# Kernel optimization log

Measured on AMD Instinct MI355X. Metric: run time of the kernel, lower is better.

## Reference

```python
import jax, jax.numpy as jnp
import numpy as np

B, T, K = 256, 512, 128


def setup_inputs() -> dict:
    key = jax.random.key(0)
    k1, k2, k3, k4 = jax.random.split(key, 4)
    logits = jax.random.normal(k1, (B, T, K), dtype=jnp.float32)
    labels = jax.random.randint(k2, (B, T), 0, K, dtype=jnp.int32)
    seq_lens = jax.random.randint(k3, (B,), 1, T + 1, dtype=jnp.int32)
    trans = jax.random.uniform(k4, (K, K), dtype=jnp.float32)
    return {"logits": logits, "labels": labels, "seq_lens": seq_lens, "trans": trans}


def _crf_neg_log_likelihood(logits, labels, seq_lens, trans):
    # logits: [B,T,K], labels: [B,T] int, seq_lens: [B] int, trans: [K,K]
    Bb, Tt, Kk = logits.shape
    mask = (jnp.arange(Tt)[None, :] < seq_lens[:, None])  # [B,T] bool

    # ---- gold sequence score ----
    unary = jnp.take_along_axis(logits, labels[..., None].astype(jnp.int32), axis=-1)[..., 0]  # [B,T]
    unary_score = jnp.sum(jnp.where(mask, unary, 0.0), axis=-1)  # [B]
    pair = trans[labels[:, :-1], labels[:, 1:]]  # [B,T-1]
    pair_score = jnp.sum(jnp.where(mask[:, 1:], pair, 0.0), axis=-1)  # [B]
    score = unary_score + pair_score  # [B]

    # ---- log partition via forward algorithm (lax.scan over time) ----
    alpha0 = logits[:, 0]  # [B,K]
    xs = (jnp.swapaxes(logits[:, 1:], 0, 1), jnp.swapaxes(mask[:, 1:], 0, 1))  # [T-1,B,K],[T-1,B]

    def step(alpha, x):
        logit_t, m_t = x
        # alpha[:, :, None] + trans[None] : [B, K_prev, K_next]
        new = jax.nn.logsumexp(alpha[:, :, None] + trans[None, :, :], axis=1) + logit_t
        alpha = jnp.where(m_t[:, None], new, alpha)
        return alpha, None

    alpha, _ = jax.lax.scan(step, alpha0, xs)
    log_z = jax.nn.logsumexp(alpha, axis=-1)  # [B]

    log_likelihood = score - log_z
    return jnp.sum(-log_likelihood)  # scalar, matches tf.reduce_sum(-ll)


def reference(logits, labels, seq_lens, trans):
    return _crf_neg_log_likelihood(logits, labels, seq_lens, trans)
```

## Files before the change

kernel.cpp:

```cpp
#include <hip/hip_runtime.h>

#define Bdim 256
#define Tdim 512
#define Kdim 128
#define NT   512

#define BAR() asm volatile("s_waitcnt lgkmcnt(0)\n\ts_barrier" ::: "memory")

template <int CTRL>
__device__ __forceinline__ float dpp_add(float v) {
    int r = __builtin_amdgcn_update_dpp(0, __float_as_int(v), CTRL, 0xF, 0xF, true);
    return v + __int_as_float(r);
}

__global__ __launch_bounds__(NT, 1) void crf_nll_kernel(
    const float* __restrict__ logits,
    const int*   __restrict__ labels,
    const int*   __restrict__ seq_lens,
    const float* __restrict__ trans,
    float* __restrict__ out)
{
    const int b   = blockIdx.x;
    const int tid = threadIdx.x;
    const int j4  = tid >> 4;
    const int g   = tid & 15;
    const int cj  = 4 * j4 + (g & 3);
    const int L   = seq_lens[b];

    __shared__ float pbuf[2][Kdim];
    __shared__ float sred[NT / 64];
    __shared__ float ared[NT / 64];

    const int*   lab_b   = labels + (size_t)b * Tdim;
    const float* logit_b = logits + (size_t)b * Tdim * Kdim;

    float e[2][4][4];
    #pragma unroll
    for (int ii = 0; ii < 2; ++ii) {
        const int f = (g << 1) + (((g >> 2) & 1) ^ ii);
        #pragma unroll
        for (int ci = 0; ci < 4; ++ci) {
            const float4 tr =
                *(const float4*)&trans[(size_t)(4 * f + ci) * Kdim + 4 * j4];
            e[ii][ci][0] = __expf(tr.x);
            e[ii][ci][1] = __expf(tr.y);
            e[ii][ci][2] = __expf(tr.z);
            e[ii][ci][3] = __expf(tr.w);
        }
    }
    #pragma unroll
    for (int ii = 0; ii < 2; ++ii)
        #pragma unroll
        for (int ci = 0; ci < 4; ++ci)
            #pragma unroll
            for (int c = 0; c < 4; ++c)
                asm volatile("" : "+v"(e[ii][ci][c]));

    float s = 0.f;
    {
        const int t = tid;
        if (t < L) {
            const int lb = lab_b[t];
            s = logit_b[(size_t)t * Kdim + lb];
            if (t >= 1) s += trans[lab_b[t - 1] * Kdim + lb];
        }
    }
    #pragma unroll
    for (int o = 32; o > 0; o >>= 1) s += __shfl_down(s, o, 64);
    if ((tid & 63) == 0) sred[tid >> 6] = s;

    float a = 0.f, off = 0.f;
    if (g < 4) {
        a = __expf(logit_b[cj]);
        pbuf[0][cj] = a;
    }
    int cb = 0;
    __syncthreads();

    float score = 0.f;
    if (tid == 0) {
        #pragma unroll
        for (int w = 0; w < NT / 64; ++w) score += sred[w];
    }

    float curl[8], nxtl[8];
    #pragma unroll
    for (int u = 0; u < 8; ++u) {
        const int tt = 1 + u;
        curl[u] = (tt < Tdim) ? logit_b[(size_t)tt * Kdim + cj] : 0.f;
    }

    for (int tb = 1; tb < L; tb += 8) {
        #pragma unroll
        for (int u = 0; u < 8; ++u) {
            const int tt = tb + 8 + u;
            nxtl[u] = (tt < Tdim) ? logit_b[(size_t)tt * Kdim + cj] : 0.f;
        }
        #pragma unroll
        for (int u = 0; u < 8; ++u) {
            const int t = tb + u;
            if (t < L) {
                const float4* p4 = (const float4*)pbuf[cb];
                const float p0  = pbuf[cb][0];
                const float lp0 = __logf(p0);
                const float sc  = __expf(curl[u] - lp0);
                float acc0 = 0.f, acc1 = 0.f, acc2 = 0.f, acc3 = 0.f;
                #pragma unroll
                for (int ii = 0; ii < 2; ++ii) {
                    const float4 p = p4[(g << 1) + (((g >> 2) & 1) ^ ii)];
                    acc0 = fmaf(p.x, e[ii][0][0], acc0);
                    acc1 = fmaf(p.x, e[ii][0][1], acc1);
                    acc2 = fmaf(p.x, e[ii][0][2], acc2);
                    acc3 = fmaf(p.x, e[ii][0][3], acc3);
                    acc0 = fmaf(p.y, e[ii][1][0], acc0);
                    acc1 = fmaf(p.y, e[ii][1][1], acc1);
                    acc2 = fmaf(p.y, e[ii][1][2], acc2);
                    acc3 = fmaf(p.y, e[ii][1][3], acc3);
                    acc0 = fmaf(p.z, e[ii][2][0], acc0);
                    acc1 = fmaf(p.z, e[ii][2][1], acc1);
                    acc2 = fmaf(p.z, e[ii][2][2], acc2);
                    acc3 = fmaf(p.z, e[ii][2][3], acc3);
                    acc0 = fmaf(p.w, e[ii][3][0], acc0);
                    acc1 = fmaf(p.w, e[ii][3][1], acc1);
                    acc2 = fmaf(p.w, e[ii][3][2], acc2);
                    acc3 = fmaf(p.w, e[ii][3][3], acc3);
                }
                off += lp0;
                acc0 = dpp_add<0xB1>(acc0); acc0 = dpp_add<0x4E>(acc0);
                acc0 = dpp_add<0x124>(acc0); acc0 = dpp_add<0x128>(acc0);
                acc1 = dpp_add<0xB1>(acc1); acc1 = dpp_add<0x4E>(acc1);
                acc1 = dpp_add<0x124>(acc1); acc1 = dpp_add<0x128>(acc1);
                acc2 = dpp_add<0xB1>(acc2); acc2 = dpp_add<0x4E>(acc2);
                acc2 = dpp_add<0x124>(acc2); acc2 = dpp_add<0x128>(acc2);
                acc3 = dpp_add<0xB1>(acc3); acc3 = dpp_add<0x4E>(acc3);
                acc3 = dpp_add<0x124>(acc3); acc3 = dpp_add<0x128>(acc3);
                float sel  = (g & 1) ? acc1 : acc0;
                float selh = (g & 1) ? acc3 : acc2;
                sel = (g & 2) ? selh : sel;
                const float anew = sel * sc;
                if (g < 4) {
                    a = anew;
                    pbuf[cb ^ 1][cj] = anew;
                }
                cb ^= 1;
                BAR();
            }
        }
        #pragma unroll
        for (int u = 0; u < 8; ++u) curl[u] = nxtl[u];
    }

    float as = (g < 4) ? a : 0.f;
    #pragma unroll
    for (int o = 32; o > 0; o >>= 1) as += __shfl_down(as, o, 64);
    if ((tid & 63) == 0) ared[tid >> 6] = as;
    __syncthreads();
    if (tid == 0) {
        float tot = 0.f;
        #pragma unroll
        for (int w = 0; w < NT / 64; ++w) tot += ared[w];
        const float logz = off + __logf(tot);
        atomicAdd(out, logz - score);
    }
}

extern "C" void kernel_launch(void* const* d_in, const int* in_sizes, int n_in,
                              void* d_out, int out_size, void* d_ws, size_t ws_size,
                              hipStream_t stream) {
    const float* logits   = (const float*)d_in[0];
    const int*   labels   = (const int*)d_in[1];
    const int*   seq_lens = (const int*)d_in[2];
    const float* trans    = (const float*)d_in[3];
    float* out = (float*)d_out;

    (void)hipMemsetAsync(out, 0, sizeof(float), stream);
    crf_nll_kernel<<<dim3(Bdim), dim3(NT), 0, stream>>>(
        logits, labels, seq_lens, trans, out);
}
```

Before: 273.3 us.

## Double block size so each thread computes two output states instead of four

Raises threads per block from 512 to 1024. Each 16-lane group now covers 2 next-states instead of 4, which halves the per-thread FMA and DPP reduction chain in every serial time step. The logit prefetch depth drops from 8 to 4 steps. In exchange, each barrier now synchronises 16 wavefronts instead of 8, shared-memory broadcast reads double, and the register-pinning asm hints are removed.

```diff
diff --git a/kernel.cpp b/kernel.cpp
--- a/kernel.cpp
+++ b/kernel.cpp
@@ -3,7 +3,7 @@
 #define Bdim 256
 #define Tdim 512
 #define Kdim 128
-#define NT   512
+#define NT   1024
 
 #define BAR() asm volatile("s_waitcnt lgkmcnt(0)\n\ts_barrier" ::: "memory")
 
@@ -22,9 +22,9 @@
 {
     const int b   = blockIdx.x;
     const int tid = threadIdx.x;
-    const int j4  = tid >> 4;
+    const int jc  = tid >> 4;
     const int g   = tid & 15;
-    const int cj  = 4 * j4 + (g & 3);
+    const int cj  = 2 * jc + (g & 1);
     const int L   = seq_lens[b];
 
     __shared__ float pbuf[2][Kdim];
@@ -34,27 +34,18 @@
     const int*   lab_b   = labels + (size_t)b * Tdim;
     const float* logit_b = logits + (size_t)b * Tdim * Kdim;
 
-    float e[2][4][4];
+    float e[2][4][2];
     #pragma unroll
     for (int ii = 0; ii < 2; ++ii) {
         const int f = (g << 1) + (((g >> 2) & 1) ^ ii);
         #pragma unroll
         for (int ci = 0; ci < 4; ++ci) {
-            const float4 tr =
-                *(const float4*)&trans[(size_t)(4 * f + ci) * Kdim + 4 * j4];
+            const float2 tr =
+                *(const float2*)&trans[(size_t)(4 * f + ci) * Kdim + 2 * jc];
             e[ii][ci][0] = __expf(tr.x);
             e[ii][ci][1] = __expf(tr.y);
-            e[ii][ci][2] = __expf(tr.z);
-            e[ii][ci][3] = __expf(tr.w);
         }
     }
-    #pragma unroll
-    for (int ii = 0; ii < 2; ++ii)
-        #pragma unroll
-        for (int ci = 0; ci < 4; ++ci)
-            #pragma unroll
-            for (int c = 0; c < 4; ++c)
-                asm volatile("" : "+v"(e[ii][ci][c]));
 
     float s = 0.f;
     {
@@ -70,7 +61,7 @@
     if ((tid & 63) == 0) sred[tid >> 6] = s;
 
     float a = 0.f, off = 0.f;
-    if (g < 4) {
+    if (g < 2) {
         a = __expf(logit_b[cj]);
         pbuf[0][cj] = a;
     }
@@ -83,62 +74,48 @@
         for (int w = 0; w < NT / 64; ++w) score += sred[w];
     }
 
-    float curl[8], nxtl[8];
+    float curl[4], nxtl[4];
     #pragma unroll
-    for (int u = 0; u < 8; ++u) {
+    for (int u = 0; u < 4; ++u) {
         const int tt = 1 + u;
         curl[u] = (tt < Tdim) ? logit_b[(size_t)tt * Kdim + cj] : 0.f;
     }
 
-    for (int tb = 1; tb < L; tb += 8) {
+    for (int tb = 1; tb < L; tb += 4) {
         #pragma unroll
-        for (int u = 0; u < 8; ++u) {
-            const int tt = tb + 8 + u;
+        for (int u = 0; u < 4; ++u) {
+            const int tt = tb + 4 + u;
             nxtl[u] = (tt < Tdim) ? logit_b[(size_t)tt * Kdim + cj] : 0.f;
         }
         #pragma unroll
-        for (int u = 0; u < 8; ++u) {
+        for (int u = 0; u < 4; ++u) {
             const int t = tb + u;
             if (t < L) {
                 const float4* p4 = (const float4*)pbuf[cb];
                 const float p0  = pbuf[cb][0];
                 const float lp0 = __logf(p0);
                 const float sc  = __expf(curl[u] - lp0);
-                float acc0 = 0.f, acc1 = 0.f, acc2 = 0.f, acc3 = 0.f;
+                float acc0 = 0.f, acc1 = 0.f;
                 #pragma unroll
                 for (int ii = 0; ii < 2; ++ii) {
                     const float4 p = p4[(g << 1) + (((g >> 2) & 1) ^ ii)];
                     acc0 = fmaf(p.x, e[ii][0][0], acc0);
                     acc1 = fmaf(p.x, e[ii][0][1], acc1);
-                    acc2 = fmaf(p.x, e[ii][0][2], acc2);
-                    acc3 = fmaf(p.x, e[ii][0][3], acc3);
                     acc0 = fmaf(p.y, e[ii][1][0], acc0);
                     acc1 = fmaf(p.y, e[ii][1][1], acc1);
-                    acc2 = fmaf(p.y, e[ii][1][2], acc2);
-                    acc3 = fmaf(p.y, e[ii][1][3], acc3);
                     acc0 = fmaf(p.z, e[ii][2][0], acc0);
                     acc1 = fmaf(p.z, e[ii][2][1], acc1);
-                    acc2 = fmaf(p.z, e[ii][2][2], acc2);
-                    acc3 = fmaf(p.z, e[ii][2][3], acc3);
                     acc0 = fmaf(p.w, e[ii][3][0], acc0);
                     acc1 = fmaf(p.w, e[ii][3][1], acc1);
-                    acc2 = fmaf(p.w, e[ii][3][2], acc2);
-                    acc3 = fmaf(p.w, e[ii][3][3], acc3);
                 }
                 off += lp0;
                 acc0 = dpp_add<0xB1>(acc0); acc0 = dpp_add<0x4E>(acc0);
                 acc0 = dpp_add<0x124>(acc0); acc0 = dpp_add<0x128>(acc0);
                 acc1 = dpp_add<0xB1>(acc1); acc1 = dpp_add<0x4E>(acc1);
                 acc1 = dpp_add<0x124>(acc1); acc1 = dpp_add<0x128>(acc1);
-                acc2 = dpp_add<0xB1>(acc2); acc2 = dpp_add<0x4E>(acc2);
-                acc2 = dpp_add<0x124>(acc2); acc2 = dpp_add<0x128>(acc2);
-                acc3 = dpp_add<0xB1>(acc3); acc3 = dpp_add<0x4E>(acc3);
-                acc3 = dpp_add<0x124>(acc3); acc3 = dpp_add<0x128>(acc3);
-                float sel  = (g & 1) ? acc1 : acc0;
-                float selh = (g & 1) ? acc3 : acc2;
-                sel = (g & 2) ? selh : sel;
+                const float sel  = (g & 1) ? acc1 : acc0;
                 const float anew = sel * sc;
-                if (g < 4) {
+                if (g < 2) {
                     a = anew;
                     pbuf[cb ^ 1][cj] = anew;
                 }
@@ -147,10 +124,10 @@
             }
         }
         #pragma unroll
-        for (int u = 0; u < 8; ++u) curl[u] = nxtl[u];
+        for (int u = 0; u < 4; ++u) curl[u] = nxtl[u];
     }
 
-    float as = (g < 4) ? a : 0.f;
+    float as = (g < 2) ? a : 0.f;
     #pragma unroll
     for (int o = 32; o > 0; o >>= 1) as += __shfl_down(as, o, 64);
     if ((tid & 63) == 0) ared[tid >> 6] = as;
```

Result: slower. 308.9 us (+13.0%).
